# Kernel tuning notes

Hardware: AMD Instinct MI355X
Metric: run time of the kernel (lower is better)

## Reference

```python
import jax, jax.numpy as jnp
import numpy as np

NUM_BINS = 15
N, C = 524288, 100


def setup_inputs() -> dict:
    key = jax.random.key(0)
    k1, k2 = jax.random.split(key)
    logits = jax.random.normal(k1, (N, C), dtype=jnp.float32)
    labels = jax.random.randint(k2, (N,), 0, C, dtype=jnp.int64)
    return {"logits": logits, "labels": labels}


def reference(logits, labels):
    # softmax over classes
    outputs = jax.nn.softmax(logits, axis=1)                      # [N, C]
    # per-sample prob of the true class and the max (confidence)
    pred_probs = jnp.take_along_axis(outputs, labels[:, None].astype(jnp.int32), axis=1)[:, 0]  # [N]
    max_probs = jnp.max(outputs, axis=1)                          # [N]
    # bin assignment: floor(p / (1/num_bins)) clamped to [0, num_bins-1]
    bin_idx = jnp.clip(jnp.floor(max_probs * NUM_BINS).astype(jnp.int32), 0, NUM_BINS - 1)
    # single-pass histogram via segment_sum (replaces per-bin masked loop)
    ones = jnp.ones_like(max_probs)
    counts = jax.ops.segment_sum(ones, bin_idx, num_segments=NUM_BINS)       # [B]
    sum_conf = jax.ops.segment_sum(max_probs, bin_idx, num_segments=NUM_BINS)
    sum_acc = jax.ops.segment_sum(pred_probs, bin_idx, num_segments=NUM_BINS)
    nonempty = counts > 0
    safe_counts = jnp.where(nonempty, counts, 1.0)
    bin_conf = jnp.where(nonempty, sum_conf / safe_counts, 0.0)
    bin_acc = jnp.where(nonempty, sum_acc / safe_counts, 0.0)
    ece = jnp.sum(counts * jnp.abs(bin_conf - bin_acc)) / jnp.sum(counts)
    return ece
```

## Files before the change

### kernel.cpp

```cpp
#include <hip/hip_runtime.h>
#include <math.h>

#define NUM_BINS 15
#define CCLS 100
#define BLOCK 256
#define GRID 1024
#define WPB (BLOCK / 64)
#define RPI 16
#define PAD 101
#define NLD 25

__global__ __launch_bounds__(BLOCK) void ece_stream(
    const float* __restrict__ logits,
    const int* __restrict__ labels,
    float* __restrict__ ws,
    float* __restrict__ out,
    int n_rows)
{
    __shared__ float s_stage[WPB][RPI * PAD];
    __shared__ float s_bin[NUM_BINS];
    __shared__ int s_last;

    const int tid  = threadIdx.x;
    const int lane = tid & 63;
    const int wave = tid >> 6;

    if (tid < NUM_BINS) s_bin[tid] = 0.f;
    __syncthreads();

    const int b  = blockIdx.x;
    const int bp = (b & 7) * (GRID / 8) + (b >> 3);
    const int gw = bp * WPB + wave;
    const int n_waves = GRID * WPB;
    const int rows_per_wave = n_rows / n_waves;
    const int iters = rows_per_wave / RPI;
    const int row_base = gw * rows_per_wave;

    float* const my_stage = s_stage[wave];
    const int q = lane >> 4;
    const int r = lane & 15;
    float* const srow = my_stage + r * PAD + 25 * q;

    float dacc_local = 0.f;
    float reg[NLD];

    {
        const float* g = logits + (size_t)row_base * CCLS;
        #pragma unroll
        for (int j = 0; j < NLD; ++j) reg[j] = g[lane + 64 * j];
    }

    for (int i = 0; i < iters; ++i) {
        const int row0 = row_base + i * RPI;

        {
            int col = lane, row_l = 0;
            #pragma unroll
            for (int j = 0; j < NLD; ++j) {
                my_stage[row_l * PAD + col] = reg[j];
                col += 64;
                if (col >= CCLS) { col -= CCLS; row_l += 1; }
            }
        }

        if (i + 1 < iters) {
            const float* g = logits + (size_t)(row0 + RPI) * CCLS;
            #pragma unroll
            for (int j = 0; j < NLD; ++j) reg[j] = g[lane + 64 * j];
        }

        const int lab = labels[row0 + r];
        float m = -1e30f, e = 0.f;
        #pragma unroll
        for (int c = 0; c < 25; ++c) {
            const float x = srow[c];
            m = fmaxf(m, x);
            e += __expf(x);
        }
        float t = 0.f;
        if ((lab >> 5 == 0 ? lab / 25 : lab / 25) == q)
            t = __expf(my_stage[r * PAD + lab]);

        #pragma unroll
        for (int off = 16; off <= 32; off <<= 1) {
            m = fmaxf(m, __shfl_xor(m, off));
            e += __shfl_xor(e, off);
            t += __shfl_xor(t, off);
        }

        if (q == 0) {
            const float inv  = 1.0f / e;
            const float conf = __expf(m) * inv;
            const float diff = conf - t * inv;
            int bin = (int)(conf * (float)NUM_BINS);
            bin = bin > NUM_BINS - 1 ? NUM_BINS - 1 : bin;
            atomicAdd(&s_bin[bin], diff);
        }
    }

    __syncthreads();
    if (tid < NUM_BINS) atomicAdd(&ws[tid], s_bin[tid]);
    __syncthreads();

    if (tid == 0) {
        __threadfence();
        const int tkt = atomicAdd((int*)(ws + 48), 1);
        s_last = (tkt == GRID - 1) ? 1 : 0;
    }
    __syncthreads();
    if (s_last && tid < 64) {
        __threadfence();
        float contrib = 0.f;
        if (tid < NUM_BINS) {
            const float v = __hip_atomic_load(&ws[tid], __ATOMIC_RELAXED, __HIP_MEMORY_SCOPE_AGENT);
            contrib = fabsf(v);
        }
        #pragma unroll
        for (int off = 32; off >= 1; off >>= 1)
            contrib += __shfl_xor(contrib, off);
        if (tid == 0) out[0] = contrib / (float)n_rows;
    }
}

extern "C" void kernel_launch(void* const* d_in, const int* in_sizes, int n_in,
                              void* d_out, int out_size, void* d_ws, size_t ws_size,
                              hipStream_t stream)
{
    const float* logits = (const float*)d_in[0];
    const int*   labels = (const int*)d_in[1];
    float* out = (float*)d_out;
    float* ws  = (float*)d_ws;

    const int n_rows = in_sizes[1];

    hipMemsetAsync(ws, 0, 64 * sizeof(float), stream);

    ece_stream<<<dim3(GRID), dim3(BLOCK), 0, stream>>>(logits, labels, ws, out, n_rows);
}
```

Before: 330.8 us.

## Stream logits tiles directly to LDS via global_load_lds double buffering

```diff
diff --git a/kernel.cpp b/kernel.cpp
--- a/kernel.cpp
+++ b/kernel.cpp
@@ -4,11 +4,22 @@
 #define NUM_BINS 15
 #define CCLS 100
 #define BLOCK 256
-#define GRID 1024
+#define GRID 768
 #define WPB (BLOCK / 64)
-#define RPI 16
-#define PAD 101
-#define NLD 25
+#define TROWS 16
+#define TFLOATS (TROWS * CCLS)
+#define NXCD 8
+
+__device__ __forceinline__ void dma16(const float* gp, float* lp) {
+    __builtin_amdgcn_global_load_lds(
+        (const __attribute__((address_space(1))) void*)gp,
+        (__attribute__((address_space(3))) void*)lp, 16, 0, 0);
+}
+__device__ __forceinline__ void dma4(const float* gp, float* lp) {
+    __builtin_amdgcn_global_load_lds(
+        (const __attribute__((address_space(1))) void*)gp,
+        (__attribute__((address_space(3))) void*)lp, 4, 0, 0);
+}
 
 __global__ __launch_bounds__(BLOCK) void ece_stream(
     const float* __restrict__ logits,
@@ -17,7 +28,7 @@
     float* __restrict__ out,
     int n_rows)
 {
-    __shared__ float s_stage[WPB][RPI * PAD];
+    __shared__ float s_buf[WPB][2][TFLOATS];
     __shared__ float s_bin[NUM_BINS];
     __shared__ int s_last;
 
@@ -29,47 +40,51 @@
     __syncthreads();
 
     const int b  = blockIdx.x;
-    const int bp = (b & 7) * (GRID / 8) + (b >> 3);
+    const int bp = (b & 7) * (GRID / NXCD) + (b >> 3);
     const int gw = bp * WPB + wave;
     const int n_waves = GRID * WPB;
-    const int rows_per_wave = n_rows / n_waves;
-    const int iters = rows_per_wave / RPI;
-    const int row_base = gw * rows_per_wave;
 
-    float* const my_stage = s_stage[wave];
+    const int ntiles = n_rows / TROWS;
+    const int tq   = ntiles / n_waves;
+    const int trem = ntiles - tq * n_waves;
+    const int nt = tq + (gw < trem ? 1 : 0);
+    const int t0 = gw * tq + (gw < trem ? gw : trem);
+
     const int q = lane >> 4;
     const int r = lane & 15;
-    float* const srow = my_stage + r * PAD + 25 * q;
 
-    float dacc_local = 0.f;
-    float reg[NLD];
+    float* cur = s_buf[wave][0];
+    float* nxt = s_buf[wave][1];
 
+    int lab_cur;
     {
-        const float* g = logits + (size_t)row_base * CCLS;
+        const float* g = logits + (size_t)t0 * TFLOATS;
         #pragma unroll
-        for (int j = 0; j < NLD; ++j) reg[j] = g[lane + 64 * j];
+        for (int k = 0; k < 6; ++k)
+            dma16(g + k * 256 + lane * 4, cur + k * 256);
+        dma4(g + 1536 + lane, cur + 1536);
+        lab_cur = labels[t0 * TROWS + r];
     }
 
-    for (int i = 0; i < iters; ++i) {
-        const int row0 = row_base + i * RPI;
+    int lab_nxt = 0;
+    for (int i = 0; i < nt; ++i) {
+        const int t = t0 + i;
 
-        {
-            int col = lane, row_l = 0;
+        if (i + 1 < nt) {
+            asm volatile("s_waitcnt lgkmcnt(0)" ::: "memory");
+            const float* g = logits + (size_t)(t + 1) * TFLOATS;
             #pragma unroll
-            for (int j = 0; j < NLD; ++j) {
-                my_stage[row_l * PAD + col] = reg[j];
-                col += 64;
-                if (col >= CCLS) { col -= CCLS; row_l += 1; }
-            }
+            for (int k = 0; k < 6; ++k)
+                dma16(g + k * 256 + lane * 4, nxt + k * 256);
+            dma4(g + 1536 + lane, nxt + 1536);
+            lab_nxt = labels[(t + 1) * TROWS + r];
+            asm volatile("s_waitcnt vmcnt(8)" ::: "memory");
+        } else {
+            asm volatile("s_waitcnt vmcnt(0)" ::: "memory");
         }
+        __builtin_amdgcn_sched_barrier(0);
 
-        if (i + 1 < iters) {
-            const float* g = logits + (size_t)(row0 + RPI) * CCLS;
-            #pragma unroll
-            for (int j = 0; j < NLD; ++j) reg[j] = g[lane + 64 * j];
-        }
-
-        const int lab = labels[row0 + r];
+        const float* srow = cur + r * CCLS + q * 25;
         float m = -1e30f, e = 0.f;
         #pragma unroll
         for (int c = 0; c < 25; ++c) {
@@ -77,25 +92,28 @@
             m = fmaxf(m, x);
             e += __expf(x);
         }
-        float t = 0.f;
-        if ((lab >> 5 == 0 ? lab / 25 : lab / 25) == q)
-            t = __expf(my_stage[r * PAD + lab]);
+        float tp = 0.f;
+        if (lab_cur / 25 == q)
+            tp = __expf(cur[r * CCLS + lab_cur]);
 
         #pragma unroll
         for (int off = 16; off <= 32; off <<= 1) {
-            m = fmaxf(m, __shfl_xor(m, off));
-            e += __shfl_xor(e, off);
-            t += __shfl_xor(t, off);
+            m  = fmaxf(m, __shfl_xor(m, off));
+            e  += __shfl_xor(e, off);
+            tp += __shfl_xor(tp, off);
         }
 
         if (q == 0) {
             const float inv  = 1.0f / e;
             const float conf = __expf(m) * inv;
-            const float diff = conf - t * inv;
+            const float diff = conf - tp * inv;
             int bin = (int)(conf * (float)NUM_BINS);
             bin = bin > NUM_BINS - 1 ? NUM_BINS - 1 : bin;
             atomicAdd(&s_bin[bin], diff);
         }
+
+        lab_cur = lab_nxt;
+        float* tmp = cur; cur = nxt; nxt = tmp;
     }
 
     __syncthreads();
@@ -112,7 +130,8 @@
         __threadfence();
         float contrib = 0.f;
         if (tid < NUM_BINS) {
-            const float v = __hip_atomic_load(&ws[tid], __ATOMIC_RELAXED, __HIP_MEMORY_SCOPE_AGENT);
+            const float v = __hip_atomic_load(&ws[tid], __ATOMIC_RELAXED,
+                                              __HIP_MEMORY_SCOPE_AGENT);
             contrib = fabsf(v);
         }
         #pragma unroll
```

Result: faster. 322.8 us (-2.4%).

## Process one row per lane with float4 loads and register bin accumulators

Applied to the files above, without the earlier changes.

```diff
diff --git a/kernel.cpp b/kernel.cpp
--- a/kernel.cpp
+++ b/kernel.cpp
@@ -6,18 +6,15 @@
 #define BLOCK 256
 #define GRID 1024
 #define WPB (BLOCK / 64)
-#define RPI 16
-#define PAD 101
-#define NLD 25
+#define NXCD 8
 
-__global__ __launch_bounds__(BLOCK) void ece_stream(
+__global__ __launch_bounds__(BLOCK, 4) void ece_rows(
     const float* __restrict__ logits,
     const int* __restrict__ labels,
     float* __restrict__ ws,
     float* __restrict__ out,
     int n_rows)
 {
-    __shared__ float s_stage[WPB][RPI * PAD];
     __shared__ float s_bin[NUM_BINS];
     __shared__ int s_last;
 
@@ -29,74 +26,62 @@
     __syncthreads();
 
     const int b  = blockIdx.x;
-    const int bp = (b & 7) * (GRID / 8) + (b >> 3);
+    const int bp = (b & 7) * (GRID / NXCD) + (b >> 3);
     const int gw = bp * WPB + wave;
     const int n_waves = GRID * WPB;
-    const int rows_per_wave = n_rows / n_waves;
-    const int iters = rows_per_wave / RPI;
-    const int row_base = gw * rows_per_wave;
+    const int rpw = n_rows / n_waves;
+    const int nit = rpw >> 6;
+    const int row_base = gw * rpw;
 
-    float* const my_stage = s_stage[wave];
-    const int q = lane >> 4;
-    const int r = lane & 15;
-    float* const srow = my_stage + r * PAD + 25 * q;
+    float acc[NUM_BINS];
+    #pragma unroll
+    for (int k = 0; k < NUM_BINS; ++k) acc[k] = 0.f;
 
-    float dacc_local = 0.f;
-    float reg[NLD];
+    for (int it = 0; it < nit; ++it) {
+        const int row = row_base + it * 64 + lane;
+        const float* rowp = logits + (size_t)row * CCLS;
+        const float4* rp = (const float4*)rowp;
+        const int lab = labels[row];
 
-    {
-        const float* g = logits + (size_t)row_base * CCLS;
+        float4 ma = make_float4(-1e30f, -1e30f, -1e30f, -1e30f);
+        float4 ea = make_float4(0.f, 0.f, 0.f, 0.f);
         #pragma unroll
-        for (int j = 0; j < NLD; ++j) reg[j] = g[lane + 64 * j];
+        for (int k = 0; k < 25; ++k) {
+            const float4 v = rp[k];
+            ma.x = fmaxf(ma.x, v.x);
+            ma.y = fmaxf(ma.y, v.y);
+            ma.z = fmaxf(ma.z, v.z);
+            ma.w = fmaxf(ma.w, v.w);
+            ea.x += __expf(v.x);
+            ea.y += __expf(v.y);
+            ea.z += __expf(v.z);
+            ea.w += __expf(v.w);
+        }
+        const float m = fmaxf(fmaxf(ma.x, ma.y), fmaxf(ma.z, ma.w));
+        const float e = (ea.x + ea.y) + (ea.z + ea.w);
+        const float xt = rowp[lab];
+
+        const float inv  = 1.0f / e;
+        const float conf = __expf(m) * inv;
+        const float diff = conf - __expf(xt) * inv;
+        int bin = (int)(conf * (float)NUM_BINS);
+        bin = bin > NUM_BINS - 1 ? NUM_BINS - 1 : bin;
+
+        #pragma unroll
+        for (int q = 0; q < NUM_BINS; ++q)
+            acc[q] += (bin == q) ? diff : 0.f;
     }
 
-    for (int i = 0; i < iters; ++i) {
-        const int row0 = row_base + i * RPI;
-
-        {
-            int col = lane, row_l = 0;
-            #pragma unroll
-            for (int j = 0; j < NLD; ++j) {
-                my_stage[row_l * PAD + col] = reg[j];
-                col += 64;
-                if (col >= CCLS) { col -= CCLS; row_l += 1; }
-            }
-        }
-
-        if (i + 1 < iters) {
-            const float* g = logits + (size_t)(row0 + RPI) * CCLS;
-            #pragma unroll
-            for (int j = 0; j < NLD; ++j) reg[j] = g[lane + 64 * j];
-        }
-
-        const int lab = labels[row0 + r];
-        float m = -1e30f, e = 0.f;
+    float mine = 0.f;
+    #pragma unroll
+    for (int q = 0; q < NUM_BINS; ++q) {
+        float v = acc[q];
         #pragma unroll
-        for (int c = 0; c < 25; ++c) {
-            const float x = srow[c];
-            m = fmaxf(m, x);
-            e += __expf(x);
-        }
-        float t = 0.f;
-        if ((lab >> 5 == 0 ? lab / 25 : lab / 25) == q)
-            t = __expf(my_stage[r * PAD + lab]);
-
-        #pragma unroll
-        for (int off = 16; off <= 32; off <<= 1) {
-            m = fmaxf(m, __shfl_xor(m, off));
-            e += __shfl_xor(e, off);
-            t += __shfl_xor(t, off);
-        }
-
-        if (q == 0) {
-            const float inv  = 1.0f / e;
-            const float conf = __expf(m) * inv;
-            const float diff = conf - t * inv;
-            int bin = (int)(conf * (float)NUM_BINS);
-            bin = bin > NUM_BINS - 1 ? NUM_BINS - 1 : bin;
-            atomicAdd(&s_bin[bin], diff);
-        }
+        for (int off = 1; off < 64; off <<= 1) v += __shfl_xor(v, off);
+        if (lane == q) mine = v;
     }
+    __syncthreads();
+    if (lane < NUM_BINS) atomicAdd(&s_bin[lane], mine);
 
     __syncthreads();
     if (tid < NUM_BINS) atomicAdd(&ws[tid], s_bin[tid]);
@@ -112,7 +97,8 @@
         __threadfence();
         float contrib = 0.f;
         if (tid < NUM_BINS) {
-            const float v = __hip_atomic_load(&ws[tid], __ATOMIC_RELAXED, __HIP_MEMORY_SCOPE_AGENT);
+            const float v = __hip_atomic_load(&ws[tid], __ATOMIC_RELAXED,
+                                              __HIP_MEMORY_SCOPE_AGENT);
             contrib = fabsf(v);
         }
         #pragma unroll
@@ -135,5 +121,5 @@
 
     hipMemsetAsync(ws, 0, 64 * sizeof(float), stream);
 
-    ece_stream<<<dim3(GRID), dim3(BLOCK), 0, stream>>>(logits, labels, ws, out, n_rows);
+    ece_rows<<<dim3(GRID), dim3(BLOCK), 0, stream>>>(logits, labels, ws, out, n_rows);
 }
```

Result: slower. 373.3 us (+12.8%).
